# Kernel tuning notes

Hardware: AMD Instinct MI355X
Metric: run time of the kernel (lower is better)

## Reference

```python
import jax, jax.numpy as jnp
import numpy as np

HIDDEN = 1024
NUM_HEADS = 16
HEAD_DIM = HIDDEN // NUM_HEADS


def setup_inputs() -> dict:
    key = jax.random.key(0)
    ks = jax.random.split(key, 5)
    scale = 1.0 / np.sqrt(HIDDEN)
    x = jax.random.normal(ks[0], (2, 2048, HIDDEN), dtype=jnp.float32)
    qkv_w = jax.random.uniform(ks[1], (3 * HIDDEN, HIDDEN), jnp.float32, -scale, scale)
    qkv_b = jax.random.uniform(ks[2], (3 * HIDDEN,), jnp.float32, -scale, scale)
    out_w = jax.random.uniform(ks[3], (HIDDEN, HIDDEN), jnp.float32, -scale, scale)
    out_b = jax.random.uniform(ks[4], (HIDDEN,), jnp.float32, -scale, scale)
    return {"x": x, "qkv_w": qkv_w, "qkv_b": qkv_b, "out_w": out_w, "out_b": out_b}


def reference(x, qkv_w, qkv_b, out_w, out_b):
    B, S, _ = x.shape
    qkv = jnp.einsum('bsd,ed->bse', x, qkv_w) + qkv_b  # [B,S,3H]
    q, k, v = jnp.split(qkv, 3, axis=-1)
    # [B,S,H] -> [B,nh,S,hd]
    def to_heads(t):
        return t.reshape(B, S, NUM_HEADS, HEAD_DIM).transpose(0, 2, 1, 3)
    q, k, v = to_heads(q), to_heads(k), to_heads(v)
    scores = jnp.einsum('bhqd,bhkd->bhqk', q, k) / np.sqrt(HEAD_DIM).astype(np.float32)
    attn = jax.nn.softmax(scores, axis=-1)
    o = jnp.einsum('bhqk,bhkd->bhqd', attn, v)
    o = o.transpose(0, 2, 1, 3).reshape(B, S, HIDDEN)
    return jnp.einsum('bsd,ed->bse', o, out_w) + out_b
```

## Files before the change

### kernel.cpp

```cpp
#include <hip/hip_runtime.h>
#include <stdint.h>

typedef __bf16 bf16x8 __attribute__((ext_vector_type(8)));
typedef float  f32x4  __attribute__((ext_vector_type(4)));
typedef float  f32x16 __attribute__((ext_vector_type(16)));
typedef unsigned short u16;
typedef unsigned int   u32;

#define B_  2
#define S_  2048
#define H_  1024
#define NH_ 16
#define HD_ 64
#define QSCL 0.18033688011112042f

__device__ __forceinline__ u16 f2bf(float f) {
  u32 u = __builtin_bit_cast(u32, f);
  return (u16)((u + 0x7FFFu + ((u >> 16) & 1u)) >> 16);
}
__device__ __forceinline__ float ex2(float x) { return __builtin_amdgcn_exp2f(x); }
__device__ __forceinline__ u32 cvtpk(float lo, float hi) {
  u32 r; asm("v_cvt_pk_bf16_f32 %0, %1, %2" : "=v"(r) : "v"(lo), "v"(hi)); return r;
}
__device__ __forceinline__ void gload_lds16(const u16* g, u16* lds) {
  __builtin_amdgcn_global_load_lds(
      (__attribute__((address_space(1))) void*)(void*)g,
      (__attribute__((address_space(3))) void*)lds, 16, 0, 0);
}
#define SBAR() asm volatile("s_barrier" ::: "memory")

__global__ void cvt_all(const float* __restrict__ a, const float* __restrict__ b,
                        const float* __restrict__ c, u16* __restrict__ oa,
                        u16* __restrict__ ob, u16* __restrict__ oc) {
  int i = blockIdx.x * 256 + threadIdx.x;
  const float4* src; ushort4* dst; int j;
  if (i < 1048576)      { src = (const float4*)a; dst = (ushort4*)oa; j = i; }
  else if (i < 1835008) { src = (const float4*)b; dst = (ushort4*)ob; j = i - 1048576; }
  else                  { src = (const float4*)c; dst = (ushort4*)oc; j = i - 1835008; }
  const float4 v = src[j];
  ushort4 o;
  o.x = f2bf(v.x); o.y = f2bf(v.y); o.z = f2bf(v.z); o.w = f2bf(v.w);
  dst[j] = o;
}

__global__ __launch_bounds__(256, 2)
void gemm_qkv(const u16* __restrict__ A, const u16* __restrict__ W,
              const float* __restrict__ bias,
              u16* __restrict__ qb, u16* __restrict__ kb, u16* __restrict__ vb)
{
  __shared__ __align__(16) u16 Al[2][128 * 64];
  __shared__ __align__(16) u16 Bl[2][192 * 64];
  const int K = 1024;
  const int tid = threadIdx.x;
  const int w = tid >> 6, l = tid & 63;
  const int lg = l >> 4, lr = l & 15;
  const int wm = w >> 1, wn = w & 1;
  const int tM = blockIdx.y * 128, tN = blockIdx.x * 192;

  f32x4 acc[4][6] = {};

  const int srow = l >> 3;
  const int scol = ((l & 7) ^ srow) << 3;
  const u16* asrc = A + (size_t)(tM + w * 32 + srow) * K + scol;
  const u16* bsrc = W + (size_t)(tN + w * 48 + srow) * K + scol;

  auto STG = [&](int buf, int k0) {
#pragma unroll
    for (int j = 0; j < 4; ++j)
      gload_lds16(asrc + (size_t)(j * 8) * K + k0, &Al[buf][(w * 32 + j * 8) * 64]);
#pragma unroll
    for (int j = 0; j < 6; ++j)
      gload_lds16(bsrc + (size_t)(j * 8) * K + k0, &Bl[buf][(w * 48 + j * 8) * 64]);
  };

  STG(0, 0);
  asm volatile("s_waitcnt vmcnt(0)" ::: "memory");
  SBAR();

  const int sw = lr & 7;

  for (int t = 0; t < 16; ++t) {
    const int cur = t & 1;
    if (t + 1 < 16) STG(cur ^ 1, (t + 1) * 64);

    bf16x8 af[4][2];
#pragma unroll
    for (int m = 0; m < 4; ++m)
#pragma unroll
      for (int kk = 0; kk < 2; ++kk)
        af[m][kk] = *(const bf16x8*)&Al[cur][(wm * 64 + m * 16 + lr) * 64 +
                                            (((kk * 4 + lg) ^ sw) << 3)];
    __builtin_amdgcn_s_setprio(1);
#pragma unroll
    for (int n = 0; n < 6; ++n) {
      bf16x8 bw0 = *(const bf16x8*)&Bl[cur][(wn * 96 + n * 16 + lr) * 64 + (((lg) ^ sw) << 3)];
      bf16x8 bw1 = *(const bf16x8*)&Bl[cur][(wn * 96 + n * 16 + lr) * 64 + (((4 + lg) ^ sw) << 3)];
#pragma unroll
      for (int m = 0; m < 4; ++m) {
        acc[m][n] = __builtin_amdgcn_mfma_f32_16x16x32_bf16(af[m][0], bw0, acc[m][n], 0, 0, 0);
        acc[m][n] = __builtin_amdgcn_mfma_f32_16x16x32_bf16(af[m][1], bw1, acc[m][n], 0, 0, 0);
      }
    }
    __builtin_amdgcn_s_setprio(0);

    asm volatile("s_waitcnt vmcnt(0)" ::: "memory");
    SBAR();
  }

#pragma unroll
  for (int n = 0; n < 6; ++n) {
    const int col = tN + wn * 96 + n * 16 + lr;
    const float bv = bias[col];
    const int t3 = col >> 10, rem = col & 1023;
    const int hh = rem >> 6, dd = rem & 63;
    const float sc = (t3 == 0) ? QSCL : 1.f;
    u16* dst = (t3 == 0) ? qb : (t3 == 1) ? kb : vb;
#pragma unroll
    for (int m = 0; m < 4; ++m)
#pragma unroll
      for (int r = 0; r < 4; ++r) {
        const int row = tM + wm * 64 + m * 16 + lg * 4 + r;
        const int bb = row >> 11, ss = row & 2047;
        dst[((size_t)(bb * NH_ + hh) * S_ + ss) * HD_ + dd] = f2bf((acc[m][n][r] + bv) * sc);
      }
  }
}

__global__ __launch_bounds__(256, 4)
void vtrans(const u16* __restrict__ vb, u16* __restrict__ vtb)
{
  __shared__ u16 Ls[64 * 65];
  const int t = threadIdx.x;
  const int bh = blockIdx.y;
  const int s0 = blockIdx.x * 64;
  const u16* src = vb + ((size_t)bh * S_ + s0) * HD_;
  const int d = t & 63, sy = t >> 6;
#pragma unroll
  for (int p = 0; p < 16; ++p) {
    const int s = p * 4 + sy;
    Ls[s * 65 + d] = src[(size_t)s * HD_ + d];
  }
  __syncthreads();
  const int s = t & 63, dy = t >> 6;
  u16* dst = vtb + (size_t)bh * HD_ * S_ + s0;
#pragma unroll
  for (int p = 0; p < 16; ++p) {
    const int dd = p * 4 + dy;
    dst[(size_t)dd * S_ + s] = Ls[s * 65 + dd];
  }
}

__global__ __launch_bounds__(256, 2)
void gemm_out(const u16* __restrict__ A, const u16* __restrict__ W,
              const float* __restrict__ bias, float* __restrict__ outf)
{
  __shared__ __align__(16) u16 Al[2][128 * 64];
  __shared__ __align__(16) u16 Bl[2][64 * 64];
  const int K = 1024, N = 1024;
  const int tid = threadIdx.x;
  const int w = tid >> 6, l = tid & 63;
  const int lg = l >> 4, lr = l & 15;
  const int tM = blockIdx.y * 128, tN = blockIdx.x * 64;

  f32x4 acc[2][4] = {};

  const int srow = l >> 3;
  const int scol = ((l & 7) ^ srow) << 3;
  const u16* asrc = A + (size_t)(tM + w * 32 + srow) * K + scol;
  const u16* bsrc = W + (size_t)(tN + w * 16 + srow) * K + scol;

  auto STG = [&](int buf, int k0) {
#pragma unroll
    for (int j = 0; j < 4; ++j)
      gload_lds16(asrc + (size_t)(j * 8) * K + k0, &Al[buf][(w * 32 + j * 8) * 64]);
#pragma unroll
    for (int j = 0; j < 2; ++j)
      gload_lds16(bsrc + (size_t)(j * 8) * K + k0, &Bl[buf][(w * 16 + j * 8) * 64]);
  };

  STG(0, 0);
  asm volatile("s_waitcnt vmcnt(0)" ::: "memory");
  SBAR();

  const int sw = lr & 7;

  for (int t = 0; t < 16; ++t) {
    const int cur = t & 1;
    if (t + 1 < 16) STG(cur ^ 1, (t + 1) * 64);

    bf16x8 af[2][2];
#pragma unroll
    for (int m = 0; m < 2; ++m)
#pragma unroll
      for (int kk = 0; kk < 2; ++kk)
        af[m][kk] = *(const bf16x8*)&Al[cur][(w * 32 + m * 16 + lr) * 64 +
                                            (((kk * 4 + lg) ^ sw) << 3)];
    __builtin_amdgcn_s_setprio(1);
#pragma unroll
    for (int n = 0; n < 4; ++n) {
      bf16x8 bw0 = *(const bf16x8*)&Bl[cur][(n * 16 + lr) * 64 + (((lg) ^ sw) << 3)];
      bf16x8 bw1 = *(const bf16x8*)&Bl[cur][(n * 16 + lr) * 64 + (((4 + lg) ^ sw) << 3)];
#pragma unroll
      for (int m = 0; m < 2; ++m) {
        acc[m][n] = __builtin_amdgcn_mfma_f32_16x16x32_bf16(af[m][0], bw0, acc[m][n], 0, 0, 0);
        acc[m][n] = __builtin_amdgcn_mfma_f32_16x16x32_bf16(af[m][1], bw1, acc[m][n], 0, 0, 0);
      }
    }
    __builtin_amdgcn_s_setprio(0);

    asm volatile("s_waitcnt vmcnt(0)" ::: "memory");
    SBAR();
  }

#pragma unroll
  for (int n = 0; n < 4; ++n) {
    const int col = tN + n * 16 + lr;
    const float bv = bias[col];
#pragma unroll
    for (int m = 0; m < 2; ++m)
#pragma unroll
      for (int r = 0; r < 4; ++r) {
        const int row = tM + w * 32 + m * 16 + lg * 4 + r;
        outf[(size_t)row * N + col] = acc[m][n][r] + bv;
      }
  }
}

__global__ __launch_bounds__(256, 2)
void attn_fwd(const u16* __restrict__ qb, const u16* __restrict__ kb,
              const u16* __restrict__ vtb, u16* __restrict__ ob)
{
  __shared__ __align__(16) u16 Kl[2][2][64 * 64];
  __shared__ __align__(16) u16 Vl[2][2][64 * 64];

  const int tid = threadIdx.x;
  const int w = tid >> 6, l = tid & 63;
  const int q32 = l & 31, hi = l >> 5;
  const int idx = blockIdx.x;
  const int bh = idx & 31, qt = idx >> 5;
  const int bb = bh >> 4, hh = bh & 15;
  const int q0 = qt * 128 + w * 32;

  bf16x8 qf[4];
#pragma unroll
  for (int ks = 0; ks < 4; ++ks)
    qf[ks] = *(const bf16x8*)&qb[((size_t)bh * S_ + q0 + q32) * HD_ + ks * 16 + hi * 8];

  const f32x16 z16 = {};
  f32x16 acc[2] = {z16, z16};
  float lrun = 0.f;

  const int srow = l >> 3;
  const int scol = ((l & 7) ^ srow) << 3;
  const u16* kbase = kb  + ((size_t)bh * S_  + w * 16 + srow) * HD_ + scol;
  const u16* vbase = vtb + ((size_t)bh * HD_ + w * 16 + srow) * S_  + scol;

  auto STAGE = [&](int buf, int t) {
#pragma unroll
    for (int s = 0; s < 2; ++s)
#pragma unroll
      for (int j = 0; j < 2; ++j) {
        gload_lds16(kbase + ((size_t)t * 128 + s * 64) * HD_ + j * 8 * HD_,
                    &Kl[buf][s][(w * 16 + j * 8) * 64]);
        gload_lds16(vbase + (size_t)t * 128 + s * 64 + j * 8 * S_,
                    &Vl[buf][s][(w * 16 + j * 8) * 64]);
      }
  };

  STAGE(0, 0);
  __syncthreads();

  const int sw = q32 & 7;

  auto SOFTMAX = [&](f32x16& st0, f32x16& st1, bf16x8* pa) {
#pragma unroll
    for (int kt = 0; kt < 2; ++kt) {
      const f32x16& stt = kt ? st1 : st0;
      float p[16];
#pragma unroll
      for (int r = 0; r < 16; ++r) p[r] = ex2(stt[r]);
#pragma unroll
      for (int g = 0; g < 4; ++g)
        lrun += (p[4 * g] + p[4 * g + 1]) + (p[4 * g + 2] + p[4 * g + 3]);
      u32 wk0[4], wk1[4];
#pragma unroll
      for (int g = 0; g < 4; ++g) {
        wk0[g] = cvtpk(p[4 * g], p[4 * g + 1]);
        wk1[g] = cvtpk(p[4 * g + 2], p[4 * g + 3]);
      }
#pragma unroll
      for (int k2 = 0; k2 < 2; ++k2) {
        u32 a0 = wk0[2 * k2], b0 = wk0[2 * k2 + 1];
        u32 a1 = wk1[2 * k2], b1 = wk1[2 * k2 + 1];
        asm volatile("v_permlane32_swap_b32 %0, %1" : "+v"(a0), "+v"(b0));
        asm volatile("v_permlane32_swap_b32 %0, %1" : "+v"(a1), "+v"(b1));
        uint4 wv = {a0, a1, b0, b1};
        pa[kt * 2 + k2] = __builtin_bit_cast(bf16x8, wv);
      }
    }
  };

  for (int t = 0; t < 16; ++t) {
    const int cur = t & 1;
    if (t + 1 < 16) STAGE(cur ^ 1, t + 1);

    f32x16 stA0 = z16, stA1 = z16, stB0 = z16, stB1 = z16;
    __builtin_amdgcn_s_setprio(1);
#pragma unroll
    for (int ks = 0; ks < 4; ++ks) {
      const int so = ((((ks << 1) | hi) ^ sw) << 3);
      const bf16x8 kfA0 = *(const bf16x8*)&Kl[cur][0][(q32) * 64 + so];
      const bf16x8 kfA1 = *(const bf16x8*)&Kl[cur][0][(32 + q32) * 64 + so];
      const bf16x8 kfB0 = *(const bf16x8*)&Kl[cur][1][(q32) * 64 + so];
      const bf16x8 kfB1 = *(const bf16x8*)&Kl[cur][1][(32 + q32) * 64 + so];
      stA0 = __builtin_amdgcn_mfma_f32_32x32x16_bf16(kfA0, qf[ks], stA0, 0, 0, 0);
      stA1 = __builtin_amdgcn_mfma_f32_32x32x16_bf16(kfA1, qf[ks], stA1, 0, 0, 0);
      stB0 = __builtin_amdgcn_mfma_f32_32x32x16_bf16(kfB0, qf[ks], stB0, 0, 0, 0);
      stB1 = __builtin_amdgcn_mfma_f32_32x32x16_bf16(kfB1, qf[ks], stB1, 0, 0, 0);
    }
    __builtin_amdgcn_s_setprio(0);

    bf16x8 pa[4];
    SOFTMAX(stA0, stA1, pa);
    __builtin_amdgcn_s_setprio(1);
#pragma unroll
    for (int dt = 0; dt < 2; ++dt)
#pragma unroll
      for (int ks = 0; ks < 4; ++ks) {
        const bf16x8 vf = *(const bf16x8*)&Vl[cur][0][(dt * 32 + q32) * 64 + ((((ks << 1) | hi) ^ sw) << 3)];
        acc[dt] = __builtin_amdgcn_mfma_f32_32x32x16_bf16(vf, pa[ks], acc[dt], 0, 0, 0);
      }
    __builtin_amdgcn_s_setprio(0);

    SOFTMAX(stB0, stB1, pa);
    __builtin_amdgcn_s_setprio(1);
#pragma unroll
    for (int dt = 0; dt < 2; ++dt)
#pragma unroll
      for (int ks = 0; ks < 4; ++ks) {
        const bf16x8 vf = *(const bf16x8*)&Vl[cur][1][(dt * 32 + q32) * 64 + ((((ks << 1) | hi) ^ sw) << 3)];
        acc[dt] = __builtin_amdgcn_mfma_f32_32x32x16_bf16(vf, pa[ks], acc[dt], 0, 0, 0);
      }
    __builtin_amdgcn_s_setprio(0);

    __syncthreads();
  }

  lrun += __shfl_xor(lrun, 32);
  const float linv = 1.f / lrun;
  const size_t orow = ((size_t)(bb * S_ + q0 + q32)) * H_ + hh * HD_;
#pragma unroll
  for (int dt = 0; dt < 2; ++dt)
#pragma unroll
    for (int g = 0; g < 4; ++g) {
      const u32 o0 = cvtpk(acc[dt][4 * g] * linv, acc[dt][4 * g + 1] * linv);
      const u32 o1 = cvtpk(acc[dt][4 * g + 2] * linv, acc[dt][4 * g + 3] * linv);
      uint2 ov; ov.x = o0; ov.y = o1;
      *(uint2*)&ob[orow + dt * 32 + g * 8 + hi * 4] = ov;
    }
}

extern "C" void kernel_launch(void* const* d_in, const int* in_sizes, int n_in,
                              void* d_out, int out_size, void* d_ws, size_t ws_size,
                              hipStream_t stream) {
  const float* x     = (const float*)d_in[0];
  const float* qkv_w = (const float*)d_in[1];
  const float* qkv_b = (const float*)d_in[2];
  const float* out_w = (const float*)d_in[3];
  const float* out_b = (const float*)d_in[4];

  char* ws = (char*)d_ws;
  u16* xb    = (u16*)(ws);
  u16* wqkvb = (u16*)(ws + 8388608);
  u16* wob   = (u16*)(ws + 14680064);
  u16* qb    = (u16*)(ws + 16777216);
  u16* kb    = (u16*)(ws + 25165824);
  u16* vb    = (u16*)(ws + 33554432);
  u16* ob    = (u16*)(ws + 41943040);
  u16* vtb   = xb;

  cvt_all<<<8192, 256, 0, stream>>>(x, qkv_w, out_w, xb, wqkvb, wob);

  gemm_qkv<<<dim3(16, 32), 256, 0, stream>>>(xb, wqkvb, qkv_b, qb, kb, vb);
  vtrans<<<dim3(32, 32), 256, 0, stream>>>(vb, vtb);
  attn_fwd<<<512, 256, 0, stream>>>(qb, kb, vtb, ob);
  gemm_out<<<dim3(16, 32), 256, 0, stream>>>(ob, wob, out_b, (float*)d_out);
}
```

Before: 105.6 us.

## Fuse V transpose into QKV GEMM epilogue via shared memory staging

The QKV GEMM epilogue now writes the V part of its tile transposed into shared memory and then stores it directly in the [b,h,d,s] layout with 16-byte stores. This removes the separate vtrans kernel, its launch, and the round trip of V through global memory. In exchange, V-producing blocks get an extra barrier and shared-memory pass, and the LDS buffers are merged into one aliased array.

Measured after the change: 98.12 us (median of 2 runs). 1.08x faster.

```diff
diff --git a/kernel.cpp b/kernel.cpp
--- a/kernel.cpp
+++ b/kernel.cpp
@@ -46,10 +46,10 @@
 __global__ __launch_bounds__(256, 2)
 void gemm_qkv(const u16* __restrict__ A, const u16* __restrict__ W,
               const float* __restrict__ bias,
-              u16* __restrict__ qb, u16* __restrict__ kb, u16* __restrict__ vb)
+              u16* __restrict__ qb, u16* __restrict__ kb, u16* __restrict__ vtb)
 {
-  __shared__ __align__(16) u16 Al[2][128 * 64];
-  __shared__ __align__(16) u16 Bl[2][192 * 64];
+  __shared__ __align__(16) u16 smem[40960];
+  u16* const Vt = smem;
   const int K = 1024;
   const int tid = threadIdx.x;
   const int w = tid >> 6, l = tid & 63;
@@ -67,10 +67,10 @@
   auto STG = [&](int buf, int k0) {
 #pragma unroll
     for (int j = 0; j < 4; ++j)
-      gload_lds16(asrc + (size_t)(j * 8) * K + k0, &Al[buf][(w * 32 + j * 8) * 64]);
+      gload_lds16(asrc + (size_t)(j * 8) * K + k0, &smem[buf * 8192 + (w * 32 + j * 8) * 64]);
 #pragma unroll
     for (int j = 0; j < 6; ++j)
-      gload_lds16(bsrc + (size_t)(j * 8) * K + k0, &Bl[buf][(w * 48 + j * 8) * 64]);
+      gload_lds16(bsrc + (size_t)(j * 8) * K + k0, &smem[16384 + buf * 12288 + (w * 48 + j * 8) * 64]);
   };
 
   STG(0, 0);
@@ -88,13 +88,13 @@
     for (int m = 0; m < 4; ++m)
 #pragma unroll
       for (int kk = 0; kk < 2; ++kk)
-        af[m][kk] = *(const bf16x8*)&Al[cur][(wm * 64 + m * 16 + lr) * 64 +
-                                            (((kk * 4 + lg) ^ sw) << 3)];
+        af[m][kk] = *(const bf16x8*)&smem[cur * 8192 + (wm * 64 + m * 16 + lr) * 64 +
+                                          (((kk * 4 + lg) ^ sw) << 3)];
     __builtin_amdgcn_s_setprio(1);
 #pragma unroll
     for (int n = 0; n < 6; ++n) {
-      bf16x8 bw0 = *(const bf16x8*)&Bl[cur][(wn * 96 + n * 16 + lr) * 64 + (((lg) ^ sw) << 3)];
-      bf16x8 bw1 = *(const bf16x8*)&Bl[cur][(wn * 96 + n * 16 + lr) * 64 + (((4 + lg) ^ sw) << 3)];
+      bf16x8 bw0 = *(const bf16x8*)&smem[16384 + cur * 12288 + (wn * 96 + n * 16 + lr) * 64 + (((lg) ^ sw) << 3)];
+      bf16x8 bw1 = *(const bf16x8*)&smem[16384 + cur * 12288 + (wn * 96 + n * 16 + lr) * 64 + (((4 + lg) ^ sw) << 3)];
 #pragma unroll
       for (int m = 0; m < 4; ++m) {
         acc[m][n] = __builtin_amdgcn_mfma_f32_16x16x32_bf16(af[m][0], bw0, acc[m][n], 0, 0, 0);
@@ -107,46 +107,48 @@
     SBAR();
   }
 
+  const int bb = tM >> 11, ssb = tM & 2047;
 #pragma unroll
   for (int n = 0; n < 6; ++n) {
-    const int col = tN + wn * 96 + n * 16 + lr;
+    const int cl = wn * 96 + n * 16 + lr;
+    const int col = tN + cl;
     const float bv = bias[col];
     const int t3 = col >> 10, rem = col & 1023;
     const int hh = rem >> 6, dd = rem & 63;
-    const float sc = (t3 == 0) ? QSCL : 1.f;
-    u16* dst = (t3 == 0) ? qb : (t3 == 1) ? kb : vb;
-#pragma unroll
-    for (int m = 0; m < 4; ++m)
-#pragma unroll
-      for (int r = 0; r < 4; ++r) {
-        const int row = tM + wm * 64 + m * 16 + lg * 4 + r;
-        const int bb = row >> 11, ss = row & 2047;
-        dst[((size_t)(bb * NH_ + hh) * S_ + ss) * HD_ + dd] = f2bf((acc[m][n][r] + bv) * sc);
-      }
-  }
-}
-
-__global__ __launch_bounds__(256, 4)
-void vtrans(const u16* __restrict__ vb, u16* __restrict__ vtb)
-{
-  __shared__ u16 Ls[64 * 65];
-  const int t = threadIdx.x;
-  const int bh = blockIdx.y;
-  const int s0 = blockIdx.x * 64;
-  const u16* src = vb + ((size_t)bh * S_ + s0) * HD_;
-  const int d = t & 63, sy = t >> 6;
-#pragma unroll
-  for (int p = 0; p < 16; ++p) {
-    const int s = p * 4 + sy;
-    Ls[s * 65 + d] = src[(size_t)s * HD_ + d];
-  }
-  __syncthreads();
-  const int s = t & 63, dy = t >> 6;
-  u16* dst = vtb + (size_t)bh * HD_ * S_ + s0;
-#pragma unroll
-  for (int p = 0; p < 16; ++p) {
-    const int dd = p * 4 + dy;
-    dst[(size_t)dd * S_ + s] = Ls[s * 65 + dd];
+    if (t3 < 2) {
+      const float sc = (t3 == 0) ? QSCL : 1.f;
+      u16* dst = (t3 == 0) ? qb : kb;
+#pragma unroll
+      for (int m = 0; m < 4; ++m)
+#pragma unroll
+        for (int r = 0; r < 4; ++r) {
+          const int row = tM + wm * 64 + m * 16 + lg * 4 + r;
+          dst[((size_t)(bb * NH_ + hh) * S_ + (row & 2047)) * HD_ + dd] = f2bf((acc[m][n][r] + bv) * sc);
+        }
+    } else {
+#pragma unroll
+      for (int m = 0; m < 4; ++m) {
+        ushort4 pk;
+        pk.x = f2bf(acc[m][n][0] + bv);
+        pk.y = f2bf(acc[m][n][1] + bv);
+        pk.z = f2bf(acc[m][n][2] + bv);
+        pk.w = f2bf(acc[m][n][3] + bv);
+        *(ushort4*)&Vt[cl * 136 + wm * 64 + m * 16 + lg * 4] = pk;
+      }
+    }
+  }
+
+  if (tN >= 1920) {
+    __syncthreads();
+    const int cl0 = (tN < 2048) ? (2048 - tN) : 0;
+    const int nch = (192 - cl0) * 16;
+    for (int c = tid; c < nch; c += 256) {
+      const int cv = cl0 + (c >> 4), ch = c & 15;
+      const int rem = (tN + cv) & 1023;
+      const int hh2 = rem >> 6, dd2 = rem & 63;
+      const uint4 v = *(const uint4*)&Vt[cv * 136 + ch * 8];
+      *(uint4*)&vtb[((size_t)(bb * NH_ + hh2) * HD_ + dd2) * S_ + ssb + ch * 8] = v;
+    }
   }
 }
 
@@ -375,14 +377,12 @@
   u16* wob   = (u16*)(ws + 14680064);
   u16* qb    = (u16*)(ws + 16777216);
   u16* kb    = (u16*)(ws + 25165824);
-  u16* vb    = (u16*)(ws + 33554432);
+  u16* vtb   = (u16*)(ws + 33554432);
   u16* ob    = (u16*)(ws + 41943040);
-  u16* vtb   = xb;
 
   cvt_all<<<8192, 256, 0, stream>>>(x, qkv_w, out_w, xb, wqkvb, wob);
 
-  gemm_qkv<<<dim3(16, 32), 256, 0, stream>>>(xb, wqkvb, qkv_b, qb, kb, vb);
-  vtrans<<<dim3(32, 32), 256, 0, stream>>>(vb, vtb);
+  gemm_qkv<<<dim3(16, 32), 256, 0, stream>>>(xb, wqkvb, qkv_b, qb, kb, vtb);
   attn_fwd<<<512, 256, 0, stream>>>(qb, kb, vtb, ob);
   gemm_out<<<dim3(16, 32), 256, 0, stream>>>(ob, wob, out_b, (float*)d_out);
 }
```
